# Kernel optimization log

Hardware: AMD Instinct MI355X
Metric: run time of the kernel (lower is better)

## Reference

```python
import jax, jax.numpy as jnp
import numpy as np

D_BINS = 59          # cfg.cam_d
BEV_H, BEV_W = 128, 128


def setup_inputs() -> dict:
    key = jax.random.key(0)
    k = jax.random.split(key, 7)
    B, N, Cin, H, W = 4, 6, 256, 16, 44
    C = 80  # cfg.cam_bev_c
    img_feats = jax.random.normal(k[0], (B, N, Cin, H, W), dtype=jnp.float32)
    rots = jax.random.normal(k[1], (B, N, 3, 3), dtype=jnp.float32)
    trans = jax.random.normal(k[2], (B, N, 3), dtype=jnp.float32)
    intrins = jax.random.normal(k[3], (B, N, 3, 3), dtype=jnp.float32)
    # 1x1 conv == per-pixel linear layer: weight (D+C, Cin), bias (D+C,)
    w_depth = jax.random.normal(k[4], (D_BINS + C, Cin), dtype=jnp.float32) / np.sqrt(Cin)
    b_depth = jnp.zeros((D_BINS + C,), dtype=jnp.float32)
    # projected BEV grid indices (what get_geometry produces via randint)
    geom = jax.random.randint(k[5], (B, N, D_BINS, H, W, 2), 0, BEV_H, dtype=jnp.int32)
    return {"img_feats": img_feats, "rots": rots, "trans": trans,
            "intrins": intrins, "w_depth": w_depth, "b_depth": b_depth,
            "geom": geom}


def reference(img_feats, rots, trans, intrins, w_depth, b_depth, geom):
    B, N, Cin, H, W = img_feats.shape
    C = w_depth.shape[0] - D_BINS
    # depth_net: 1x1 conv -> (B, N, D+C, H, W)
    x = jnp.einsum('bnchw,oc->bnohw', img_feats, w_depth) + b_depth[None, None, :, None, None]
    depth = jax.nn.softmax(x[:, :, :D_BINS], axis=2)          # (B,N,D,H,W)
    context = x[:, :, D_BINS:]                                 # (B,N,C,H,W)
    # outer product: (B,N,D,C,H,W) -> (B,N,D,H,W,C)
    frustum = depth[:, :, :, None] * context[:, :, None]
    frustum = jnp.transpose(frustum, (0, 1, 2, 4, 5, 3))
    # voxel pooling: scatter-add frustum points into BEV grid by geom indices
    cell = geom[..., 0] * BEV_W + geom[..., 1]                 # (B,N,D,H,W)
    flat_idx = (jnp.arange(B, dtype=jnp.int32)[:, None] * (BEV_H * BEV_W)
                + cell.reshape(B, -1)).reshape(-1)
    bev = jax.ops.segment_sum(frustum.reshape(-1, C), flat_idx,
                              num_segments=B * BEV_H * BEV_W)
    return bev.reshape(B, BEV_H, BEV_W, C).transpose(0, 3, 1, 2)  # (B,C,bev_h,bev_w)
```

## Files before the change

kernel.cpp:

```cpp
#include <hip/hip_runtime.h>
#include <hip/hip_bf16.h>
#include <math.h>

#define D_BINS 59
#define CTX    80
#define O_TOT  139
#define K_CIN  256
#define PIXELS 704
#define BNPAIR 24
#define BEVHW  16384
#define NBATCH 4

#define NTILE   128
#define NBUCKET (NBATCH * NTILE)
#define TCELLS  128

#define PXT    16
#define NPXT   44
#define NBLK   (BNPAIR * NPXT)
#define SEGS   (6 * NPXT)
#define EPB    (PXT * D_BINS)

#define CAP    2816
#define CAPP   (CAP + TCELLS * 7)

#define WHL_OFF      0
#define WHL_F        36864
#define CTX_OFF      (WHL_OFF + WHL_F)
#define CTX_F        (BNPAIR * PIXELS * CTX / 2)
#define CNTMAT_OFF   (CTX_OFF + CTX_F)
#define OFSMAT_OFF   (CNTMAT_OFF + NTILE * NBLK)
#define PLIST_OFF    (OFSMAT_OFF + NTILE * NBLK)

typedef __attribute__((ext_vector_type(8))) short bf16x8;
typedef __attribute__((ext_vector_type(4))) float f32x4;

__device__ __forceinline__ unsigned short f2bf(float v) {
    __hip_bfloat16 h = __float2bfloat16(v);
    return *reinterpret_cast<unsigned short*>(&h);
}
__device__ __forceinline__ float bf2f(unsigned short u) {
    return __uint_as_float(((unsigned)u) << 16);
}

__global__ __launch_bounds__(256) void wsplit_kernel(
    const float* __restrict__ w, unsigned short* __restrict__ whl)
{
    const int row = blockIdx.x;
    const int col = threadIdx.x;
    const float v = (row < O_TOT) ? w[(size_t)row * K_CIN + col] : 0.f;
    const unsigned short hi = f2bf(v);
    const unsigned short lo = f2bf(v - bf2f(hi));
    whl[row * K_CIN + col]         = hi;
    whl[36864 + row * K_CIN + col] = lo;
}

template<int NT, int T0>
__device__ __forceinline__ void kloop(
    const float* __restrict__ ib, const unsigned short* __restrict__ whl,
    int pxg, int m, int g, f32x4* acc)
{
#pragma unroll 2
    for (int ks = 0; ks < 8; ++ks) {
        float bv[8];
#pragma unroll
        for (int j = 0; j < 8; ++j)
            bv[j] = ib[(size_t)(ks * 32 + 8 * g + j) * PIXELS + pxg];
        bf16x8 bhi, blo;
#pragma unroll
        for (int j = 0; j < 8; ++j) {
            const unsigned short h = f2bf(bv[j]);
            bhi[j] = (short)h;
            blo[j] = (short)f2bf(bv[j] - bf2f(h));
        }
#pragma unroll
        for (int t = 0; t < NT; ++t) {
            const int row = (T0 + t) * 16 + m;
            const bf16x8 ahi = *(const bf16x8*)&whl[(size_t)row * K_CIN + ks * 32 + g * 8];
            const bf16x8 alo = *(const bf16x8*)&whl[36864 + (size_t)row * K_CIN + ks * 32 + g * 8];
            acc[t] = __builtin_amdgcn_mfma_f32_16x16x32_bf16(ahi, bhi, acc[t], 0, 0, 0);
            acc[t] = __builtin_amdgcn_mfma_f32_16x16x32_bf16(ahi, blo, acc[t], 0, 0, 0);
            acc[t] = __builtin_amdgcn_mfma_f32_16x16x32_bf16(alo, bhi, acc[t], 0, 0, 0);
        }
    }
}

__global__ __launch_bounds__(64) void gemm_fused(
    const float* __restrict__ img,
    const unsigned short* __restrict__ whl,
    const float* __restrict__ bias,
    const int*   __restrict__ geom,
    __hip_bfloat16* __restrict__ ctx,
    uint2*       __restrict__ plist,
    int*         __restrict__ cntmat_t,
    int*         __restrict__ ofsmat_t)
{
    const int lane = threadIdx.x;
    const int m    = lane & 15;
    const int g    = lane >> 4;
    const int pt   = blockIdx.x;
    const int bn   = blockIdx.y;
    const int p0   = pt * PXT;
    const int pxg  = p0 + m;
    const int blkid = bn * NPXT + pt;
    const float* ib = img + (size_t)bn * K_CIN * PIXELS;

    if (blockIdx.z == 0) {
        __shared__ int lh[NTILE], lofs[NTILE], lcur[NTILE];
        f32x4 acc[4];
#pragma unroll
        for (int t = 0; t < 4; ++t) acc[t] = (f32x4){0.f, 0.f, 0.f, 0.f};
        kloop<4, 0>(ib, whl, pxg, m, g, acc);

        const int2* g2 = (const int2*)geom;
        int2 gg[4][4];
#pragma unroll
        for (int t = 0; t < 4; ++t)
#pragma unroll
            for (int r = 0; r < 4; ++r) {
                const int o = 16 * t + 4 * g + r;
                if (o < D_BINS)
                    gg[t][r] = g2[((size_t)(bn * D_BINS + o)) * PIXELS + pxg];
            }
        lh[lane] = 0; lh[lane + 64] = 0;
        lcur[lane] = 0; lcur[lane + 64] = 0;

#pragma unroll
        for (int t = 0; t < 4; ++t)
#pragma unroll
            for (int r = 0; r < 4; ++r) acc[t][r] += bias[16 * t + 4 * g + r];

        float gm = -INFINITY;
#pragma unroll
        for (int t = 0; t < 4; ++t)
#pragma unroll
            for (int r = 0; r < 4; ++r)
                if (16 * t + 4 * g + r < D_BINS) gm = fmaxf(gm, acc[t][r]);
        gm = fmaxf(gm, __shfl_xor(gm, 16));
        gm = fmaxf(gm, __shfl_xor(gm, 32));
        float ls = 0.f;
#pragma unroll
        for (int t = 0; t < 4; ++t)
#pragma unroll
            for (int r = 0; r < 4; ++r)
                if (16 * t + 4 * g + r < D_BINS) {
                    const float e = __expf(acc[t][r] - gm);
                    acc[t][r] = e;
                    ls += e;
                }
        ls += __shfl_xor(ls, 16);
        ls += __shfl_xor(ls, 32);
        const float inv = 1.f / ls;

        unsigned uc[4][4];
#pragma unroll
        for (int t = 0; t < 4; ++t)
#pragma unroll
            for (int r = 0; r < 4; ++r) {
                const int o = 16 * t + 4 * g + r;
                if (o < D_BINS) {
                    const int2 q = gg[t][r];
                    const int tile = (q.x >> 3) * 8 + (q.y >> 4);
                    const int cell = (q.x & 7) * 16 + (q.y & 15);
                    uc[t][r] = (unsigned)((tile << 7) | cell);
                    atomicAdd(&lh[tile], 1);
                }
            }

        const int l2 = 2 * lane;
        const int a = lh[l2];
        const int b = lh[l2 + 1];
        const int p = a + b;
        int incl = p;
#pragma unroll
        for (int off = 1; off < 64; off <<= 1) {
            const int t = __shfl_up(incl, off);
            if (lane >= off) incl += t;
        }
        const int excl = incl - p;
        lofs[l2]     = excl;
        lofs[l2 + 1] = excl + a;
        cntmat_t[(size_t)l2 * NBLK + blkid]       = a;
        cntmat_t[(size_t)(l2 + 1) * NBLK + blkid] = b;
        ofsmat_t[(size_t)l2 * NBLK + blkid]       = excl;
        ofsmat_t[(size_t)(l2 + 1) * NBLK + blkid] = excl + a;

        uint2* dst = plist + (size_t)blkid * EPB;
        const unsigned ctxoff = (unsigned)((bn * PIXELS + pxg) * CTX);
#pragma unroll
        for (int t = 0; t < 4; ++t)
#pragma unroll
            for (int r = 0; r < 4; ++r) {
                const int o = 16 * t + 4 * g + r;
                if (o < D_BINS) {
                    const unsigned u = uc[t][r];
                    const int tl = (int)(u >> 7);
                    const int pos = lofs[tl] + atomicAdd(&lcur[tl], 1);
                    dst[pos] = make_uint2(__float_as_uint(acc[t][r] * inv),
                                          (ctxoff << 7) | (u & 127u));
                }
            }
    } else {
        __shared__ unsigned short sctx[PXT][CTX];
        f32x4 acc[6];
#pragma unroll
        for (int t = 0; t < 6; ++t) acc[t] = (f32x4){0.f, 0.f, 0.f, 0.f};
        kloop<6, 3>(ib, whl, pxg, m, g, acc);

#pragma unroll
        for (int t = 0; t < 6; ++t)
#pragma unroll
            for (int r = 0; r < 4; ++r) {
                const int o = (3 + t) * 16 + 4 * g + r;
                const int c = o - D_BINS;
                if (c >= 0 && c < CTX)
                    sctx[m][c] = f2bf(acc[t][r] + bias[o]);
            }
        const char* sb = (const char*)sctx;
        char* gb = (char*)ctx + ((size_t)(bn * PIXELS) + p0) * CTX * 2;
#pragma unroll
        for (int i = lane; i < PXT * CTX * 2 / 16; i += 64)
            *(float4*)(gb + i * 16) = *(const float4*)(sb + i * 16);
    }
}

__global__ __launch_bounds__(1024) void gather_kernel(
    const uint2* __restrict__ plist,
    const int*   __restrict__ cntmat_t,
    const int*   __restrict__ ofsmat_t,
    const unsigned short* __restrict__ ctx,
    float*       __restrict__ out)
{
    __shared__ float sacc[CTX][TCELLS + 1];
    __shared__ uint2 bufB[CAPP];
    __shared__ int segcnt[SEGS], segofsL[SEGS], segofsG[SEGS];
    __shared__ int cellcnt[TCELLS], celloff[TCELLS], cellcur[TCELLS];
    __shared__ int sTotal;
    uint2* bufA = (uint2*)sacc;

    const int tid    = threadIdx.x;
    const int wv     = tid >> 6;
    const int lane   = tid & 63;
    const int bucket = blockIdx.x;
    const int b      = bucket >> 7;
    const int tile   = bucket & 127;
    const int blk0   = b * SEGS;

    if (tid < SEGS) {
        segcnt[tid]  = cntmat_t[(size_t)tile * NBLK + blk0 + tid];
        segofsG[tid] = ofsmat_t[(size_t)tile * NBLK + blk0 + tid];
    }
    if (tid >= 512 && tid < 512 + TCELLS) cellcnt[tid - 512] = 0;
    __syncthreads();

    if (wv == 0) {
        int carry = 0;
#pragma unroll
        for (int c = 0; c < 5; ++c) {
            const int i = c * 64 + lane;
            const int v = (i < SEGS) ? segcnt[i] : 0;
            int incl = v;
#pragma unroll
            for (int off = 1; off < 64; off <<= 1) {
                const int t = __shfl_up(incl, off);
                if (lane >= off) incl += t;
            }
            if (i < SEGS) segofsL[i] = carry + incl - v;
            carry += __shfl(incl, 63);
        }
        if (lane == 0) sTotal = carry;
    }
    __syncthreads();
    const int total = sTotal;
    const int ncap  = (total < CAP) ? total : CAP;

    {
        const int sub = lane >> 3;
        const int sl  = lane & 7;
        for (int sgi = wv * 8 + sub; sgi < SEGS; sgi += 128) {
            const int n = segcnt[sgi];
            if (!n) continue;
            const int dstb = segofsL[sgi];
            const uint2* sp = plist + (size_t)(blk0 + sgi) * EPB + segofsG[sgi];
            for (int i = sl; i < n; i += 8) {
                const int d = dstb + i;
                if (d < CAP) {
                    const uint2 e = sp[i];
                    bufA[d] = e;
                    atomicAdd(&cellcnt[e.y & 127u], 1);
                }
            }
        }
    }
    __syncthreads();

    if (wv == 1) {
        int carry = 0;
#pragma unroll
        for (int c = 0; c < 2; ++c) {
            const int i = c * 64 + lane;
            const int pv = (cellcnt[i] + 7) & ~7;
            int incl = pv;
#pragma unroll
            for (int off = 1; off < 64; off <<= 1) {
                const int t = __shfl_up(incl, off);
                if (lane >= off) incl += t;
            }
            celloff[i] = carry + incl - pv;
            cellcur[i] = 0;
            carry += __shfl(incl, 63);
        }
    }
    __syncthreads();

    if (tid < TCELLS) {
        const int o = celloff[tid] + cellcnt[tid];
        const int e = celloff[tid] + ((cellcnt[tid] + 7) & ~7);
        for (int i = o; i < e; ++i) bufB[i] = make_uint2(0u, 0u);
    }
    for (int i = tid; i < ncap; i += 1024) {
        const uint2 e = bufA[i];
        const int c = (int)(e.y & 127u);
        bufB[celloff[c] + atomicAdd(&cellcur[c], 1)] = e;
    }
    __syncthreads();

    for (int c = wv; c < TCELLS; c += 16) {
        const int s0 = celloff[c];
        const int pc = (cellcnt[c] + 7) & ~7;
        float a0 = 0.f, a1 = 0.f;
        for (int i = 0; i < pc; i += 8) {
            uint2 e[8];
#pragma unroll
            for (int r = 0; r < 8; ++r) e[r] = bufB[s0 + i + r];
            if (lane < 40) {
                unsigned u[8];
#pragma unroll
                for (int r = 0; r < 8; ++r)
                    u[r] = *(const unsigned*)(ctx + (e[r].y >> 7) + 2 * lane);
#pragma unroll
                for (int r = 0; r < 8; ++r) {
                    const float d  = __uint_as_float(e[r].x);
                    a0 += d * __uint_as_float(u[r] << 16);
                    a1 += d * __uint_as_float(u[r] & 0xffff0000u);
                }
            }
        }
        if (lane < 40) {
            sacc[2 * lane][c]     = a0;
            sacc[2 * lane + 1][c] = a1;
        }
    }

    if (total > CAP) {
        for (int sgi = 0; sgi < SEGS; ++sgi) {
            const int dstb = segofsL[sgi];
            const int n    = segcnt[sgi];
            if (dstb + n <= CAP) continue;
            const uint2* sp = plist + (size_t)(blk0 + sgi) * EPB + segofsG[sgi];
            const int i0 = (CAP > dstb) ? (CAP - dstb) : 0;
            for (int i = i0; i < n; ++i) {
                const uint2 e = sp[i];
                const int c = (int)(e.y & 127u);
                if ((c & 15) == wv && lane < 40) {
                    const unsigned u = *(const unsigned*)(ctx + (e.y >> 7) + 2 * lane);
                    const float dep = __uint_as_float(e.x);
                    sacc[2 * lane][c]     += dep * __uint_as_float(u << 16);
                    sacc[2 * lane + 1][c] += dep * __uint_as_float(u & 0xffff0000u);
                }
            }
        }
    }
    __syncthreads();

    const int tr = tile >> 3;
    const int tc = tile & 7;
    const int c0  = tid >> 4;
    const int col = tid & 15;
#pragma unroll
    for (int cc = c0; cc < CTX; cc += 64) {
#pragma unroll
        for (int r = 0; r < 8; ++r) {
            out[((size_t)(b * CTX + cc)) * BEVHW + (tr * 8 + r) * 128 + tc * 16 + col]
                = sacc[cc][r * 16 + col];
        }
    }
}

extern "C" void kernel_launch(void* const* d_in, const int* in_sizes, int n_in,
                              void* d_out, int out_size, void* d_ws, size_t ws_size,
                              hipStream_t stream)
{
    const float* img  = (const float*)d_in[0];
    const float* w    = (const float*)d_in[4];
    const float* bias = (const float*)d_in[5];
    const int*   geom = (const int*)d_in[6];
    float*       out  = (float*)d_out;

    float* ws = (float*)d_ws;
    unsigned short* whl = (unsigned short*)(ws + WHL_OFF);
    __hip_bfloat16* ctx = (__hip_bfloat16*)(ws + CTX_OFF);
    int*   cntmat_t = (int*)(ws + CNTMAT_OFF);
    int*   ofsmat_t = (int*)(ws + OFSMAT_OFF);
    uint2* plist    = (uint2*)(ws + PLIST_OFF);

    wsplit_kernel<<<144, 256, 0, stream>>>(w, whl);

    {
        dim3 grid(NPXT, BNPAIR, 2);
        gemm_fused<<<grid, 64, 0, stream>>>(img, whl, bias, geom, ctx,
                                            plist, cntmat_t, ofsmat_t);
    }

    gather_kernel<<<NBUCKET, 1024, 0, stream>>>(plist, cntmat_t, ofsmat_t,
                                                (const unsigned short*)ctx, out);
}
```

Measured before the change: 140.9 us.

## Pre-split image into bf16 hi/lo MFMA fragment layout in a prep kernel

Adds a prep kernel that converts image features into bf16 hi/lo pairs and stores them in the exact per-lane MFMA fragment layout, with the weights also reordered into fragment order. The GEMM then loads contiguous 16-byte vectors instead of doing strided fp32 loads and per-element splitting, and the split work is no longer duplicated across the two z-blocks. In exchange it writes and rereads an extra image-sized workspace buffer, and the prep kernel adds a pass over the image.

```diff
diff --git a/kernel.cpp b/kernel.cpp
--- a/kernel.cpp
+++ b/kernel.cpp
@@ -24,13 +24,15 @@
 #define CAP    2816
 #define CAPP   (CAP + TCELLS * 7)
 
-#define WHL_OFF      0
-#define WHL_F        36864
-#define CTX_OFF      (WHL_OFF + WHL_F)
-#define CTX_F        (BNPAIR * PIXELS * CTX / 2)
-#define CNTMAT_OFF   (CTX_OFF + CTX_F)
-#define OFSMAT_OFF   (CNTMAT_OFF + NTILE * NBLK)
-#define PLIST_OFF    (OFSMAT_OFF + NTILE * NBLK)
+#define WHLF_OFF   0
+#define WHLF_F     36864
+#define IMGF_OFF   (WHLF_OFF + WHLF_F)
+#define IMGF_F     (NBLK * 4096)
+#define CTX_OFF    (IMGF_OFF + IMGF_F)
+#define CTX_F      (BNPAIR * PIXELS * CTX / 2)
+#define CNTMAT_OFF (CTX_OFF + CTX_F)
+#define OFSMAT_OFF (CNTMAT_OFF + NTILE * NBLK)
+#define PLIST_OFF  (OFSMAT_OFF + NTILE * NBLK)
 
 typedef __attribute__((ext_vector_type(8))) short bf16x8;
 typedef __attribute__((ext_vector_type(4))) float f32x4;
@@ -43,41 +45,71 @@
     return __uint_as_float(((unsigned)u) << 16);
 }
 
-__global__ __launch_bounds__(256) void wsplit_kernel(
-    const float* __restrict__ w, unsigned short* __restrict__ whl)
+__global__ __launch_bounds__(256) void prep_kernel(
+    const float* __restrict__ img,
+    const float* __restrict__ w,
+    unsigned short* __restrict__ wf,
+    unsigned short* __restrict__ imgf)
 {
-    const int row = blockIdx.x;
-    const int col = threadIdx.x;
-    const float v = (row < O_TOT) ? w[(size_t)row * K_CIN + col] : 0.f;
-    const unsigned short hi = f2bf(v);
-    const unsigned short lo = f2bf(v - bf2f(hi));
-    whl[row * K_CIN + col]         = hi;
-    whl[36864 + row * K_CIN + col] = lo;
+    const int tid = threadIdx.x;
+    if (blockIdx.x == NPXT) {
+#pragma unroll
+        for (int i = 0; i < 6; ++i) {
+            const int row = blockIdx.y * 6 + i;
+            const int col = tid;
+            const float v = (row < O_TOT) ? w[(size_t)row * K_CIN + col] : 0.f;
+            const unsigned short hi = f2bf(v);
+            const unsigned short lo = f2bf(v - bf2f(hi));
+            const int t = row >> 4, m = row & 15;
+            const int ks = col >> 5, kk = col & 31;
+            const int g = kk >> 3, e = kk & 7;
+            const size_t base = (size_t)(t * 8 + ks) * 1024 + (g * 16 + m) * 8 + e;
+            wf[base]       = hi;
+            wf[base + 512] = lo;
+        }
+        return;
+    }
+    __shared__ unsigned short sf[8192];
+    const int pt = blockIdx.x, bn = blockIdx.y;
+    const int blk = bn * NPXT + pt;
+    const float* ib = img + (size_t)bn * K_CIN * PIXELS + pt * PXT;
+#pragma unroll
+    for (int half = 0; half < 2; ++half) {
+        const int eid = half * 256 + tid;
+        const int kk = eid >> 4, px = eid & 15;
+#pragma unroll
+        for (int ks = 0; ks < 8; ++ks) {
+            const float v = ib[(size_t)(ks * 32 + kk) * PIXELS + px];
+            const unsigned short hi = f2bf(v);
+            const unsigned short lo = f2bf(v - bf2f(hi));
+            const int g = kk >> 3, e = kk & 7;
+            sf[ks * 1024 + (g * 16 + px) * 8 + e]       = hi;
+            sf[ks * 1024 + 512 + (g * 16 + px) * 8 + e] = lo;
+        }
+    }
+    __syncthreads();
+    uint2* ob = (uint2*)(imgf + (size_t)blk * 8192);
+    const uint2* sb = (const uint2*)sf;
+#pragma unroll
+    for (int i = 0; i < 8; ++i)
+        ob[tid + 256 * i] = sb[tid + 256 * i];
 }
 
 template<int NT, int T0>
 __device__ __forceinline__ void kloop(
-    const float* __restrict__ ib, const unsigned short* __restrict__ whl,
-    int pxg, int m, int g, f32x4* acc)
+    const unsigned short* __restrict__ ifr,
+    const unsigned short* __restrict__ wf,
+    int lane, f32x4* acc)
 {
 #pragma unroll 2
     for (int ks = 0; ks < 8; ++ks) {
-        float bv[8];
-#pragma unroll
-        for (int j = 0; j < 8; ++j)
-            bv[j] = ib[(size_t)(ks * 32 + 8 * g + j) * PIXELS + pxg];
-        bf16x8 bhi, blo;
-#pragma unroll
-        for (int j = 0; j < 8; ++j) {
-            const unsigned short h = f2bf(bv[j]);
-            bhi[j] = (short)h;
-            blo[j] = (short)f2bf(bv[j] - bf2f(h));
-        }
+        const bf16x8 bhi = *(const bf16x8*)&ifr[ks * 1024 + lane * 8];
+        const bf16x8 blo = *(const bf16x8*)&ifr[ks * 1024 + 512 + lane * 8];
 #pragma unroll
         for (int t = 0; t < NT; ++t) {
-            const int row = (T0 + t) * 16 + m;
-            const bf16x8 ahi = *(const bf16x8*)&whl[(size_t)row * K_CIN + ks * 32 + g * 8];
-            const bf16x8 alo = *(const bf16x8*)&whl[36864 + (size_t)row * K_CIN + ks * 32 + g * 8];
+            const size_t ab = (size_t)((T0 + t) * 8 + ks) * 1024 + lane * 8;
+            const bf16x8 ahi = *(const bf16x8*)&wf[ab];
+            const bf16x8 alo = *(const bf16x8*)&wf[ab + 512];
             acc[t] = __builtin_amdgcn_mfma_f32_16x16x32_bf16(ahi, bhi, acc[t], 0, 0, 0);
             acc[t] = __builtin_amdgcn_mfma_f32_16x16x32_bf16(ahi, blo, acc[t], 0, 0, 0);
             acc[t] = __builtin_amdgcn_mfma_f32_16x16x32_bf16(alo, bhi, acc[t], 0, 0, 0);
@@ -86,8 +118,8 @@
 }
 
 __global__ __launch_bounds__(64) void gemm_fused(
-    const float* __restrict__ img,
-    const unsigned short* __restrict__ whl,
+    const unsigned short* __restrict__ imgf,
+    const unsigned short* __restrict__ wf,
     const float* __restrict__ bias,
     const int*   __restrict__ geom,
     __hip_bfloat16* __restrict__ ctx,
@@ -103,14 +135,14 @@
     const int p0   = pt * PXT;
     const int pxg  = p0 + m;
     const int blkid = bn * NPXT + pt;
-    const float* ib = img + (size_t)bn * K_CIN * PIXELS;
+    const unsigned short* ifr = imgf + (size_t)blkid * 8192;
 
     if (blockIdx.z == 0) {
         __shared__ int lh[NTILE], lofs[NTILE], lcur[NTILE];
         f32x4 acc[4];
 #pragma unroll
         for (int t = 0; t < 4; ++t) acc[t] = (f32x4){0.f, 0.f, 0.f, 0.f};
-        kloop<4, 0>(ib, whl, pxg, m, g, acc);
+        kloop<4, 0>(ifr, wf, lane, acc);
 
         const int2* g2 = (const int2*)geom;
         int2 gg[4][4];
@@ -205,7 +237,7 @@
         f32x4 acc[6];
 #pragma unroll
         for (int t = 0; t < 6; ++t) acc[t] = (f32x4){0.f, 0.f, 0.f, 0.f};
-        kloop<6, 3>(ib, whl, pxg, m, g, acc);
+        kloop<6, 3>(ifr, wf, lane, acc);
 
 #pragma unroll
         for (int t = 0; t < 6; ++t)
@@ -398,17 +430,21 @@
     float*       out  = (float*)d_out;
 
     float* ws = (float*)d_ws;
-    unsigned short* whl = (unsigned short*)(ws + WHL_OFF);
+    unsigned short* wf   = (unsigned short*)(ws + WHLF_OFF);
+    unsigned short* imgf = (unsigned short*)(ws + IMGF_OFF);
     __hip_bfloat16* ctx = (__hip_bfloat16*)(ws + CTX_OFF);
     int*   cntmat_t = (int*)(ws + CNTMAT_OFF);
     int*   ofsmat_t = (int*)(ws + OFSMAT_OFF);
     uint2* plist    = (uint2*)(ws + PLIST_OFF);
 
-    wsplit_kernel<<<144, 256, 0, stream>>>(w, whl);
+    {
+        dim3 grid(NPXT + 1, BNPAIR);
+        prep_kernel<<<grid, 256, 0, stream>>>(img, w, wf, imgf);
+    }
 
     {
         dim3 grid(NPXT, BNPAIR, 2);
-        gemm_fused<<<grid, 64, 0, stream>>>(img, whl, bias, geom, ctx,
+        gemm_fused<<<grid, 64, 0, stream>>>(imgf, wf, bias, geom, ctx,
                                             plist, cntmat_t, ofsmat_t);
     }
 
```

After: 138.7 us. No clear change (-1.5%).
